# Kernel tuning notes

Measured on AMD Instinct MI355X. Metric: run time of the kernel, lower is better.

The kernel has to match this reference:

```python
import jax, jax.numpy as jnp
import numpy as np

MEMORY_SIZE = 32768
DIM_K = 256
DIM_V = 256
B = 2048
OLD_SIZE = 16384


def setup_inputs() -> dict:
    key = jax.random.key(0)
    k1, k2, k3, k4, k5 = jax.random.split(key, 5)
    return {
        "q": jax.random.normal(k1, (B, DIM_K), dtype=jnp.float32),
        "k": jax.random.normal(k2, (B, DIM_K), dtype=jnp.float32),
        "v": jax.random.normal(k3, (B, DIM_V), dtype=jnp.float32),
        "K_cache": jax.random.normal(k4, (MEMORY_SIZE, DIM_K), dtype=jnp.float32),
        "V_cache": jax.random.normal(k5, (MEMORY_SIZE, DIM_V), dtype=jnp.float32),
        "old_size": OLD_SIZE,
    }


def reference(q, k, v, K_cache, V_cache, old_size):
    b, dim_k = q.shape
    new_size = old_size + b  # static python int
    # write the new chunk of keys/values into the cache
    K = jax.lax.dynamic_update_slice(K_cache, k, (old_size, 0))
    V = jax.lax.dynamic_update_slice(V_cache, v, (old_size, 0))
    Kv = K[:new_size]  # [new_size, dim_k]
    Vv = V[:new_size]  # [new_size, dim_v]
    # scaled dot-product scores: [b, new_size]
    scores = (q @ Kv.T) * (1.0 / (dim_k ** 0.5))
    # causal mask: query i (global pos old_size+i) may attend keys j <= old_size+i
    key_idx = jnp.arange(new_size)[None, :]
    query_idx = jnp.arange(old_size, new_size)[:, None]
    scores = jnp.where(key_idx > query_idx, -jnp.inf, scores)
    p = jax.nn.softmax(scores, axis=-1)
    return p @ Vv  # [b, dim_v]
```

## Files before the change

kernel.cpp:

```cpp
#include <hip/hip_runtime.h>
#include <hip/hip_bf16.h>
#include <cstdint>

typedef __attribute__((ext_vector_type(8)))  short s8b;
typedef __attribute__((ext_vector_type(4)))  short s4b;
typedef __attribute__((ext_vector_type(16))) float f16v;
typedef __attribute__((ext_vector_type(4)))  unsigned u4v;

#define MFMA32(a,b,c) __builtin_amdgcn_mfma_f32_32x32x16_bf16((a),(b),(c),0,0,0)

#define OLDN   16384
#define NEWB   2048
#define DHEAD  256
#define NTOTAL 18432
#define NTILES 576
#define EXPSC  0.09016844005556021f

static __device__ __forceinline__ short f2bf(float f) {
    unsigned u = __float_as_uint(f);
    unsigned r = (u + 0x7fffu + ((u >> 16) & 1u)) >> 16;
    return (short)r;
}
static __device__ __forceinline__ int slot_key(int s) {
    return (s & 3) + 8 * ((s >> 2) & 1) + 4 * ((s >> 3) & 1) + 16 * (s >> 4);
}

static __device__ __forceinline__ void dma16(const void* g, void* l) {
    __builtin_amdgcn_global_load_lds((const __attribute__((address_space(1))) unsigned int*)g,
                                     (__attribute__((address_space(3))) unsigned int*)l,
                                     16, 0, 0);
}

__global__ void cvt_kernel(const float* __restrict__ Kc, const float* __restrict__ kn,
                           const float* __restrict__ Vc, const float* __restrict__ vn,
                           s8b* __restrict__ Ksw, s8b* __restrict__ Vsw) {
    const int t   = blockIdx.x;
    const int tid = threadIdx.x;
    if (blockIdx.y == 0) {
#pragma unroll
        for (int i = 0; i < 4; ++i) {
            int chunk = tid + 256 * i;
            int l = chunk & 63;
            int b = chunk >> 6;
            int row = 32 * t + (l & 31);
            int col = 16 * b + 8 * (l >> 5);
            const float* src = (row < OLDN) ? Kc + (size_t)row * DHEAD + col
                                            : kn + (size_t)(row - OLDN) * DHEAD + col;
            float4 f0 = *(const float4*)src;
            float4 f1 = *(const float4*)(src + 4);
            s8b o;
            o[0]=f2bf(f0.x); o[1]=f2bf(f0.y); o[2]=f2bf(f0.z); o[3]=f2bf(f0.w);
            o[4]=f2bf(f1.x); o[5]=f2bf(f1.y); o[6]=f2bf(f1.z); o[7]=f2bf(f1.w);
            Ksw[(size_t)t * 1024 + chunk] = o;
        }
    } else {
#pragma unroll
        for (int i = 0; i < 4; ++i) {
            int chunk = tid + 256 * i;
            int l = chunk & 63;
            int b = chunk >> 6;
            int m = 32 * (b >> 1) + (l & 31);
            int sbase = 16 * (b & 1) + 8 * (l >> 5);
            s8b o;
#pragma unroll
            for (int j = 0; j < 8; ++j) {
                int row = 32 * t + slot_key(sbase + j);
                float v = (row < OLDN) ? Vc[(size_t)row * DHEAD + m]
                                       : vn[(size_t)(row - OLDN) * DHEAD + m];
                o[j] = f2bf(v);
            }
            Vsw[(size_t)t * 1024 + chunk] = o;
        }
    }
}

__global__ __launch_bounds__(256, 2)
void attn_kernel(const float* __restrict__ q,
                 const s8b* __restrict__ Ksw, const s8b* __restrict__ Vsw,
                 short* __restrict__ OPb, float* __restrict__ L, int SPLIT) {
    __shared__ short smem[2 * 16384];

    const int bx   = blockIdx.x;
    const int s    = bx % SPLIT;
    const int qb   = bx / SPLIT;
    const int q0   = qb * 128;
    const int tid  = threadIdx.x;
    const int w    = tid >> 6;
    const int lane = tid & 63;
    const int lc   = lane & 31;
    const int h    = lane >> 5;

    s8b qf[16];
    {
        const int qrow = q0 + 32 * w + lc;
        const float* qp = q + (size_t)qrow * DHEAD + 8 * h;
#pragma unroll
        for (int c = 0; c < 16; ++c) {
            float4 f0 = *(const float4*)(qp + 16 * c);
            float4 f1 = *(const float4*)(qp + 16 * c + 4);
            s8b o;
            o[0]=f2bf(f0.x*EXPSC); o[1]=f2bf(f0.y*EXPSC); o[2]=f2bf(f0.z*EXPSC); o[3]=f2bf(f0.w*EXPSC);
            o[4]=f2bf(f1.x*EXPSC); o[5]=f2bf(f1.y*EXPSC); o[6]=f2bf(f1.z*EXPSC); o[7]=f2bf(f1.w*EXPSC);
            qf[c] = o;
        }
    }

    f16v acc[8];
#pragma unroll
    for (int c = 0; c < 8; ++c)
#pragma unroll
        for (int r = 0; r < 16; ++r) acc[c][r] = 0.f;
    float lsum = 0.f;

    const int nt_total = (OLDN + q0 + 128) >> 5;
    const int tb  = nt_total / SPLIT;
    const int rem = nt_total % SPLIT;
    const int t0  = s * tb + (s < rem ? s : rem);
    const int tcnt = tb + (s < rem ? 1 : 0);
    const int tend = t0 + tcnt;
    const int qbase = OLDN + q0 + 32 * w;

    const s8b* gseg = (w < 2) ? (Ksw + (size_t)(8 * w) * 64 + lane)
                              : (Vsw + (size_t)(8 * (w - 2)) * 64 + lane);
    short* lseg = &smem[(8 * w) * 512 + lane * 8];

    {
        const s8b* g0 = gseg + (size_t)t0 * 1024;
#pragma unroll
        for (int i = 0; i < 8; ++i) dma16(g0 + i * 64, lseg + i * 512);
        const int t1 = (t0 + 1 < tend) ? t0 + 1 : t0;
        const s8b* g1 = gseg + (size_t)t1 * 1024;
#pragma unroll
        for (int i = 0; i < 8; ++i) dma16(g1 + i * 64, lseg + 16384 + i * 512);
    }
    __syncthreads();

    int cur = 0;
    for (int t = t0; t < tend; ++t, cur ^= 1) {
        const int kk = t << 5;
        const short* Kbuf = &smem[cur * 16384 + lane * 8];
        const short* Vbuf = Kbuf + 8192;

        f16v sacc0, sacc1;
#pragma unroll
        for (int r = 0; r < 16; ++r) { sacc0[r] = 0.f; sacc1[r] = 0.f; }
#pragma unroll
        for (int c = 0; c < 8; ++c) {
            s8b k0 = *(const s8b*)(Kbuf + (2 * c) * 512);
            s8b k1 = *(const s8b*)(Kbuf + (2 * c + 1) * 512);
            sacc0 = MFMA32(k0, qf[2 * c],     sacc0);
            sacc1 = MFMA32(k1, qf[2 * c + 1], sacc1);
        }

        const bool domask = (kk + 31 > qbase);
        unsigned pk[8];
#pragma unroll
        for (int i = 0; i < 8; ++i) {
            const int r0 = 2 * i, r1 = 2 * i + 1;
            float ev0 = __builtin_exp2f(sacc0[r0] + sacc1[r0]);
            float ev1 = __builtin_exp2f(sacc0[r1] + sacc1[r1]);
            if (domask) {
                if (kk + (r0 & 3) + 8 * (r0 >> 2) + 4 * h > qbase + lc) ev0 = 0.f;
                if (kk + (r1 & 3) + 8 * (r1 >> 2) + 4 * h > qbase + lc) ev1 = 0.f;
            }
            lsum += ev0 + ev1;
            pk[i] = __builtin_amdgcn_perm(__float_as_uint(ev1), __float_as_uint(ev0), 0x07060302u);
        }
        s8b pf0 = __builtin_bit_cast(s8b, (u4v){pk[0], pk[1], pk[2], pk[3]});
        s8b pf1 = __builtin_bit_cast(s8b, (u4v){pk[4], pk[5], pk[6], pk[7]});

#pragma unroll
        for (int c = 0; c < 8; ++c) {
            s8b v0 = *(const s8b*)(Vbuf + (2 * c) * 512);
            s8b v1 = *(const s8b*)(Vbuf + (2 * c + 1) * 512);
            acc[c] = MFMA32(v0, pf0, acc[c]);
            acc[c] = MFMA32(v1, pf1, acc[c]);
        }

        __syncthreads();

        {
            const int tp = (t + 2 < tend) ? t + 2 : tend - 1;
            const s8b* gp = gseg + (size_t)tp * 1024;
            short* lp = lseg + cur * 16384;
#pragma unroll
            for (int i = 0; i < 8; ++i) dma16(gp + i * 64, lp + i * 512);
        }
    }

    lsum += __shfl_xor(lsum, 32);

    const int qrow = q0 + 32 * w + lc;
    const size_t sbase = (size_t)s * NEWB;
    short* op_row = OPb + (sbase + qrow) * DHEAD;
#pragma unroll
    for (int c = 0; c < 8; ++c)
#pragma unroll
        for (int g = 0; g < 4; ++g) {
            s4b o4;
            o4[0] = f2bf(acc[c][4 * g]);
            o4[1] = f2bf(acc[c][4 * g + 1]);
            o4[2] = f2bf(acc[c][4 * g + 2]);
            o4[3] = f2bf(acc[c][4 * g + 3]);
            *(s4b*)(op_row + 32 * c + 8 * g + 4 * h) = o4;
        }
    if (h == 0) L[sbase + qrow] = lsum;
}

__global__ void combine_kernel(const short* __restrict__ OPb, const float* __restrict__ L,
                               float* __restrict__ out, int SPLIT) {
    const int row = blockIdx.x;
    const int col = threadIdx.x;
    float num = 0.f, den = 0.f;
    for (int s = 0; s < SPLIT; ++s) {
        size_t r = (size_t)s * NEWB + row;
        unsigned u = (unsigned)(unsigned short)OPb[r * DHEAD + col];
        num += __uint_as_float(u << 16);
        den += L[r];
    }
    out[(size_t)row * DHEAD + col] = num / den;
}

extern "C" void kernel_launch(void* const* d_in, const int* in_sizes, int n_in,
                              void* d_out, int out_size, void* d_ws, size_t ws_size,
                              hipStream_t stream) {
    const float* q  = (const float*)d_in[0];
    const float* kn = (const float*)d_in[1];
    const float* vn = (const float*)d_in[2];
    const float* Kc = (const float*)d_in[3];
    const float* Vc = (const float*)d_in[4];
    float* out = (float*)d_out;

    char* ws = (char*)d_ws;
    const size_t KB_BYTES = (size_t)NTOTAL * DHEAD * 2;
    s8b* Ksw = (s8b*)(ws);
    s8b* Vsw = (s8b*)(ws + KB_BYTES);
    const size_t PART_BASE = 2 * KB_BYTES;

    const size_t per_split = (size_t)NEWB * DHEAD * 2 + (size_t)NEWB * 4;
    size_t avail = (ws_size > PART_BASE) ? (ws_size - PART_BASE) : 0;
    int SPLIT = (int)(avail / per_split);
    if (SPLIT > 32) SPLIT = 32;
    if (SPLIT < 1)  SPLIT = 1;

    short* OPb = (short*)(ws + PART_BASE);
    float* L   = (float*)(ws + PART_BASE + (size_t)SPLIT * NEWB * DHEAD * 2);

    cvt_kernel<<<dim3(NTILES, 2), 256, 0, stream>>>(Kc, kn, Vc, vn, Ksw, Vsw);
    attn_kernel<<<16 * SPLIT, 256, 0, stream>>>(q, Ksw, Vsw, OPb, L, SPLIT);
    combine_kernel<<<NEWB, 256, 0, stream>>>(OPb, L, out, SPLIT);
}
```

Baseline: 168.6 us.

## Software-pipeline QK and PV MFMAs across tiles with triple-buffered V in LDS

```diff
diff --git a/kernel.cpp b/kernel.cpp
--- a/kernel.cpp
+++ b/kernel.cpp
@@ -78,7 +78,7 @@
 void attn_kernel(const float* __restrict__ q,
                  const s8b* __restrict__ Ksw, const s8b* __restrict__ Vsw,
                  short* __restrict__ OPb, float* __restrict__ L, int SPLIT) {
-    __shared__ short smem[2 * 16384];
+    __shared__ __align__(16) short smem[5 * 8192];
 
     const int bx   = blockIdx.x;
     const int s    = bx % SPLIT;
@@ -120,38 +120,22 @@
     const int tend = t0 + tcnt;
     const int qbase = OLDN + q0 + 32 * w;
 
-    const s8b* gseg = (w < 2) ? (Ksw + (size_t)(8 * w) * 64 + lane)
-                              : (Vsw + (size_t)(8 * (w - 2)) * 64 + lane);
-    short* lseg = &smem[(8 * w) * 512 + lane * 8];
-
-    {
-        const s8b* g0 = gseg + (size_t)t0 * 1024;
-#pragma unroll
-        for (int i = 0; i < 8; ++i) dma16(g0 + i * 64, lseg + i * 512);
-        const int t1 = (t0 + 1 < tend) ? t0 + 1 : t0;
-        const s8b* g1 = gseg + (size_t)t1 * 1024;
-#pragma unroll
-        for (int i = 0; i < 8; ++i) dma16(g1 + i * 64, lseg + 16384 + i * 512);
-    }
-    __syncthreads();
-
-    int cur = 0;
-    for (int t = t0; t < tend; ++t, cur ^= 1) {
-        const int kk = t << 5;
-        const short* Kbuf = &smem[cur * 16384 + lane * 8];
-        const short* Vbuf = Kbuf + 8192;
-
-        f16v sacc0, sacc1;
-#pragma unroll
-        for (int r = 0; r < 16; ++r) { sacc0[r] = 0.f; sacc1[r] = 0.f; }
-#pragma unroll
-        for (int c = 0; c < 8; ++c) {
-            s8b k0 = *(const s8b*)(Kbuf + (2 * c) * 512);
-            s8b k1 = *(const s8b*)(Kbuf + (2 * c + 1) * 512);
-            sacc0 = MFMA32(k0, qf[2 * c],     sacc0);
-            sacc1 = MFMA32(k1, qf[2 * c + 1], sacc1);
-        }
-
+    const bool isK  = (w < 2);
+    const int  seg  = isK ? (8 * w) * 512 : (8 * (w - 2)) * 512;
+    const s8b* gbase = isK ? (Ksw + (size_t)(8 * w) * 64 + lane)
+                           : (Vsw + (size_t)(8 * (w - 2)) * 64 + lane);
+    const int loff = lane * 8;
+
+    auto stage = [&](int tt) {
+        const s8b* g = gbase + (size_t)tt * 1024;
+        short* dst = isK ? (smem + (tt & 1) * 8192 + seg + loff)
+                         : (smem + 16384 + (tt % 3) * 8192 + seg + loff);
+#pragma unroll
+        for (int i = 0; i < 8; ++i) dma16(g + i * 64, dst + i * 512);
+    };
+
+    s8b pf0, pf1;
+    auto softmax_pack = [&](const f16v& sacc0, const f16v& sacc1, int kk) {
         const bool domask = (kk + 31 > qbase);
         unsigned pk[8];
 #pragma unroll
@@ -166,25 +150,61 @@
             lsum += ev0 + ev1;
             pk[i] = __builtin_amdgcn_perm(__float_as_uint(ev1), __float_as_uint(ev0), 0x07060302u);
         }
-        s8b pf0 = __builtin_bit_cast(s8b, (u4v){pk[0], pk[1], pk[2], pk[3]});
-        s8b pf1 = __builtin_bit_cast(s8b, (u4v){pk[4], pk[5], pk[6], pk[7]});
-
+        pf0 = __builtin_bit_cast(s8b, (u4v){pk[0], pk[1], pk[2], pk[3]});
+        pf1 = __builtin_bit_cast(s8b, (u4v){pk[4], pk[5], pk[6], pk[7]});
+    };
+
+    stage(t0);
+    stage(t0 + 1 < tend ? t0 + 1 : tend - 1);
+    __syncthreads();
+
+    {
+        const short* kb = smem + (t0 & 1) * 8192 + loff;
+        f16v s0, s1;
+#pragma unroll
+        for (int r = 0; r < 16; ++r) { s0[r] = 0.f; s1[r] = 0.f; }
 #pragma unroll
         for (int c = 0; c < 8; ++c) {
-            s8b v0 = *(const s8b*)(Vbuf + (2 * c) * 512);
-            s8b v1 = *(const s8b*)(Vbuf + (2 * c + 1) * 512);
+            s8b k0 = *(const s8b*)(kb + (2 * c) * 512);
+            s8b k1 = *(const s8b*)(kb + (2 * c + 1) * 512);
+            s0 = MFMA32(k0, qf[2 * c],     s0);
+            s1 = MFMA32(k1, qf[2 * c + 1], s1);
+        }
+        softmax_pack(s0, s1, t0 << 5);
+        __syncthreads();
+        stage(t0 + 2 < tend ? t0 + 2 : tend - 1);
+    }
+
+    for (int t = t0 + 1; t < tend; ++t) {
+        const short* kb = smem + (t & 1) * 8192 + loff;
+        const short* vb = smem + 16384 + ((t - 1) % 3) * 8192 + loff;
+        f16v s0, s1;
+#pragma unroll
+        for (int r = 0; r < 16; ++r) { s0[r] = 0.f; s1[r] = 0.f; }
+#pragma unroll
+        for (int c = 0; c < 8; ++c) {
+            s8b k0 = *(const s8b*)(kb + (2 * c) * 512);
+            s8b v0 = *(const s8b*)(vb + (2 * c) * 512);
+            s8b k1 = *(const s8b*)(kb + (2 * c + 1) * 512);
+            s8b v1 = *(const s8b*)(vb + (2 * c + 1) * 512);
+            s0 = MFMA32(k0, qf[2 * c], s0);
+            acc[c] = MFMA32(v0, pf0, acc[c]);
+            s1 = MFMA32(k1, qf[2 * c + 1], s1);
+            acc[c] = MFMA32(v1, pf1, acc[c]);
+        }
+        softmax_pack(s0, s1, t << 5);
+        __syncthreads();
+        stage(t + 2 < tend ? t + 2 : tend - 1);
+    }
+
+    {
+        const short* vb = smem + 16384 + ((tend - 1) % 3) * 8192 + loff;
+#pragma unroll
+        for (int c = 0; c < 8; ++c) {
+            s8b v0 = *(const s8b*)(vb + (2 * c) * 512);
+            s8b v1 = *(const s8b*)(vb + (2 * c + 1) * 512);
             acc[c] = MFMA32(v0, pf0, acc[c]);
             acc[c] = MFMA32(v1, pf1, acc[c]);
-        }
-
-        __syncthreads();
-
-        {
-            const int tp = (t + 2 < tend) ? t + 2 : tend - 1;
-            const s8b* gp = gseg + (size_t)tp * 1024;
-            short* lp = lseg + cur * 16384;
-#pragma unroll
-            for (int i = 0; i < 8; ++i) dma16(gp + i * 64, lp + i * 512);
         }
     }
 
```

Measured after the change: 172.4 us. 2.3% more time.
